# Performance work log

Hardware: AMD Instinct MI355X
Metric: run time of the kernel (lower is better)

Reference implementation:

```python
import jax, jax.numpy as jnp
import numpy as np

VERY_NEGATIVE_NUMBER = -1e30


def setup_inputs() -> dict:
    key = jax.random.key(0)
    ks = jax.random.split(key, 7)
    B, N, M, D = 16, 1024, 1024, 128
    inv_sqrt_d = 1.0 / np.sqrt(D).astype(np.float32)
    query = jax.random.normal(ks[0], (B, N, D), jnp.float32)
    memory = jax.random.normal(ks[1], (B, M, D), jnp.float32)
    # trilinear similarity parameters (BiDAF)
    w_q = jax.random.normal(ks[2], (D,), jnp.float32) * inv_sqrt_d
    w_m = jax.random.normal(ks[3], (D,), jnp.float32) * inv_sqrt_d
    w_qm = jax.random.normal(ks[4], (D,), jnp.float32) * inv_sqrt_d
    query_mask = jax.random.randint(ks[5], (B, N), 0, 2, jnp.int32)
    memory_mask = jax.random.randint(ks[6], (B, M), 0, 2, jnp.int32)
    return {
        "query": query,
        "memory": memory,
        "w_q": w_q,
        "w_m": w_m,
        "w_qm": w_qm,
        "query_mask": query_mask,
        "memory_mask": memory_mask,
    }


def reference(query, memory, w_q, w_m, w_qm, query_mask, memory_mask):
    # trilinear similarity: sim[b,n,m] = w_q.q_n + w_m.m_m + sum_d w_qm_d * q_nd * m_md
    sim = (
        jnp.einsum("bnd,d->bn", query, w_q)[:, :, None]
        + jnp.einsum("bmd,d->bm", memory, w_m)[:, None, :]
        + jnp.einsum("bnd,d,bmd->bnm", query, w_qm, memory)
    )  # [B, N, M]
    mask = (
        query_mask[:, :, None].astype(sim.dtype)
        * memory_mask[:, None, :].astype(sim.dtype)
    )  # [B, N, M]
    sim = sim + (1.0 - mask) * VERY_NEGATIVE_NUMBER
    # query -> memory attention (row-wise softmax over memory axis)
    q2m_prob = jax.nn.softmax(sim, axis=-1)  # [B, N, M]
    query_memory_attention = jnp.einsum("bnm,bmd->bnd", q2m_prob, memory)
    # memory -> query attention (softmax over row maxima, one vector per batch)
    m2q_prob = jax.nn.softmax(jnp.max(sim, axis=-1), axis=-1)  # [B, N]
    m2q = jnp.einsum("bn,bnd->bd", m2q_prob, query)[:, None, :]  # [B, 1, D]
    memory_query_attention = jnp.broadcast_to(m2q, query_memory_attention.shape)
    return (query_memory_attention, memory_query_attention)
```

## Files before the change

kernel.cpp:

```cpp
#include <hip/hip_runtime.h>
#include <hip/hip_bf16.h>
#include <stdint.h>

#define BB 16
#define NN 1024
#define MM 1024
#define DD 128
#define VERY_NEG (-1e30f)
#define LOG2E 1.44269504f
#define HALF_M 512
#define NCH 8

using bf16x8 = __attribute__((ext_vector_type(8))) short;
using f32x4  = __attribute__((ext_vector_type(4))) float;

__device__ inline unsigned short f2bf(float f) {
    union { float f; uint32_t u; } cv; cv.f = f;
    uint32_t u = cv.u;
    return (unsigned short)((u + 0x7FFFu + ((u >> 16) & 1u)) >> 16);
}
#define EXP2F(x) __builtin_amdgcn_exp2f(x)

typedef __attribute__((address_space(3))) unsigned int lds_u32;
typedef const __attribute__((address_space(1))) unsigned int glb_u32;
__device__ __forceinline__ void gl16(const void* g, void* l) {
    __builtin_amdgcn_global_load_lds((glb_u32*)g, (lds_u32*)l, 16, 0, 0);
}

__global__ void prep_rows(const float* __restrict__ q, const float* __restrict__ mem,
                          const float* __restrict__ wq, const float* __restrict__ wm,
                          const float* __restrict__ wqm, const int* __restrict__ mmask,
                          float* __restrict__ a, float* __restrict__ c1s,
                          unsigned short* __restrict__ qp, unsigned short* __restrict__ mb)
{
    int wave = (blockIdx.x * 256 + threadIdx.x) >> 6;
    int lane = threadIdx.x & 63;
    bool is_q = wave < BB * NN;
    int row = is_q ? wave : wave - BB * NN;
    const float* src = (is_q ? q : mem) + (size_t)row * DD;
    const float* wd  = is_q ? wq : wm;
    float2 v  = *(const float2*)(src + lane * 2);
    float2 w2 = *(const float2*)(wd + lane * 2);
    float dot = v.x * w2.x + v.y * w2.y;
    #pragma unroll
    for (int o = 32; o; o >>= 1) dot += __shfl_xor(dot, o);
    if (lane == 0) {
        if (is_q) a[row] = dot;
        else {
            int mm = mmask[row];
            c1s[row] = (dot + (mm ? 0.f : VERY_NEG)) * LOG2E;
        }
    }
    float2 s2 = v;
    if (is_q) {
        float2 wv = *(const float2*)(wqm + lane * 2);
        s2.x *= wv.x * LOG2E; s2.y *= wv.y * LOG2E;
    }
    ushort2 o2; o2.x = f2bf(s2.x); o2.y = f2bf(s2.y);
    *(ushort2*)((is_q ? qp : mb) + (size_t)row * DD + lane * 2) = o2;
}

__global__ void transpose_mem(const float* __restrict__ mem, unsigned short* __restrict__ mt)
{
    __shared__ unsigned short t[64][72];
    int bid = blockIdx.x;
    int dt = bid & 1, mtile = (bid >> 1) & 15, b = bid >> 5;
    int d0 = dt * 64, m0 = mtile * 64;
    int tid = threadIdx.x;
    int cc = tid & 63, rr = tid >> 6;
    #pragma unroll
    for (int r = 0; r < 64; r += 4) {
        float v = mem[((size_t)b * MM + m0 + r + rr) * DD + d0 + cc];
        t[cc][r + rr] = f2bf(v);
    }
    __syncthreads();
    #pragma unroll
    for (int r = 0; r < 64; r += 4) {
        mt[((size_t)b * DD + d0 + r + rr) * MM + m0 + cc] = t[r + rr][cc];
    }
}

__global__ __launch_bounds__(512) void flash_fwd(
    const unsigned short* __restrict__ qp, const unsigned short* __restrict__ mb,
    const unsigned short* __restrict__ mt,
    const float* __restrict__ a, const float* __restrict__ c1s,
    const int* __restrict__ qmask,
    float* __restrict__ out1, float* __restrict__ rowmax)
{
    __shared__ __align__(16) char smem[155648];
    unsigned short* KbBase = (unsigned short*)smem;
    unsigned short* VbBase = (unsigned short*)(smem + 65536);
    unsigned short (*pl)[16][72] = (unsigned short(*)[16][72])(smem + 131072);
    float* c1L = (float*)(smem + 149504);
    float (*mlb)[16][2] = (float(*)[16][2])(smem + 153600);
    float (*Obuf)[16][130] = (float(*)[16][130])smem;

    int tid = threadIdx.x;
    int w = tid >> 6, lane = tid & 63;
    int qt = w & 3, mh = w >> 2;
    int g = lane >> 4, qi = lane & 15;
    int b = blockIdx.x >> 4, nt = blockIdx.x & 15;
    int n0q = nt * 64 + qt * 16;

    const unsigned short* mbB = mb + (size_t)b * MM * DD;
    const unsigned short* mtB = mt + (size_t)b * DD * MM;

    {
        float2 cv = *(const float2*)(c1s + b * MM + tid * 2);
        *(float2*)&c1L[tid * 2] = cv;
    }

    const unsigned short* qpb = qp + ((size_t)b * NN + n0q) * DD;
    bf16x8 qf[4];
    #pragma unroll
    for (int kc = 0; kc < 4; kc++)
        qf[kc] = *(const bf16x8*)(qpb + qi * DD + kc * 32 + g * 8);

    float a_q = a[b * NN + n0q + qi];
    int   qm  = qmask[b * NN + n0q + qi];

    float m_run = -INFINITY, l_run = 0.f;
    f32x4 o[8];
    #pragma unroll
    for (int d2 = 0; d2 < 8; d2++) o[d2] = (f32x4){0.f, 0.f, 0.f, 0.f};

    auto stage = [&](int m0, unsigned short* Kc, unsigned short* Vc) {
        #pragma unroll
        for (int i = 0; i < 8; i++) {
            int j = qt * 8 + i;
            if (j < 16) {
                const unsigned short* gsrc = mbB
                    + (size_t)(m0 + (j >> 2) * 16 + (lane & 15)) * DD
                    + (j & 3) * 32 + (lane >> 4) * 8;
                gl16(gsrc, Kc + j * 512);
            } else {
                int j2 = j - 16;
                const unsigned short* gsrc = mtB
                    + (size_t)((j2 >> 1) * 16 + (lane & 15)) * MM
                    + m0 + (j2 & 1) * 32 + (lane >> 4) * 8;
                gl16(gsrc, Vc + j2 * 512);
            }
        }
    };
    auto Kbuf = [&](int bufi) { return KbBase + (mh * 2 + bufi) * 8192; };
    auto Vbuf = [&](int bufi) { return VbBase + (mh * 2 + bufi) * 8192; };

    stage(mh * HALF_M, Kbuf(0), Vbuf(0));
    __syncthreads();

    int cur = 0;
    for (int ch = 0; ch < NCH; ch++) {
        int m0 = mh * HALF_M + ch * 64;
        if (ch + 1 < NCH)
            stage(m0 + 64, Kbuf(cur ^ 1), Vbuf(cur ^ 1));

        const unsigned short* Kc = Kbuf(cur);
        const unsigned short* Vc = Vbuf(cur);

        f32x4 st[4];
        #pragma unroll
        for (int t = 0; t < 4; t++) st[t] = (f32x4){0, 0, 0, 0};
        #pragma unroll
        for (int t = 0; t < 4; t++) {
            #pragma unroll
            for (int kc = 0; kc < 4; kc++) {
                bf16x8 af = *(const bf16x8*)(Kc + ((t * 4 + kc) * 64 + lane) * 8);
                st[t] = __builtin_amdgcn_mfma_f32_16x16x32_bf16(af, qf[kc], st[t], 0, 0, 0);
            }
        }
        float sv[4][4];
        float cmax = -INFINITY;
        #pragma unroll
        for (int t = 0; t < 4; t++) {
            float4 c1v = *(const float4*)&c1L[m0 + t * 16 + g * 4];
            float cc4[4] = {c1v.x, c1v.y, c1v.z, c1v.w};
            #pragma unroll
            for (int i = 0; i < 4; i++) {
                float s = qm ? (st[t][i] + cc4[i]) : 0.f;
                sv[t][i] = s;
                cmax = fmaxf(cmax, s);
            }
        }
        cmax = fmaxf(cmax, __shfl_xor(cmax, 16));
        cmax = fmaxf(cmax, __shfl_xor(cmax, 32));
        float m_new = fmaxf(m_run, cmax);
        float alpha = EXP2F(m_run - m_new);
        float psum = 0.f;
        #pragma unroll
        for (int t = 0; t < 4; t++) {
            unsigned short pe[4];
            #pragma unroll
            for (int i = 0; i < 4; i++) {
                float p = EXP2F(sv[t][i] - m_new);
                psum += p;
                pe[i] = f2bf(p);
            }
            ushort4 pw2; pw2.x = pe[0]; pw2.y = pe[1]; pw2.z = pe[2]; pw2.w = pe[3];
            *(ushort4*)(&pl[w][qi][t * 16 + g * 4]) = pw2;
        }
        psum += __shfl_xor(psum, 16);
        psum += __shfl_xor(psum, 32);
        l_run = l_run * alpha + psum;
        m_run = m_new;

        float aL[4];
        #pragma unroll
        for (int i = 0; i < 4; i++) aL[i] = __shfl(alpha, g * 4 + i);

        __builtin_amdgcn_sched_barrier(0);
        bf16x8 pa0 = *(const bf16x8*)(&pl[w][qi][g * 8]);
        bf16x8 pa1 = *(const bf16x8*)(&pl[w][qi][32 + g * 8]);
        #pragma unroll
        for (int d2 = 0; d2 < 8; d2++) {
            bf16x8 vf0 = *(const bf16x8*)(Vc + ((d2 * 2 + 0) * 64 + lane) * 8);
            bf16x8 vf1 = *(const bf16x8*)(Vc + ((d2 * 2 + 1) * 64 + lane) * 8);
            f32x4 oo = o[d2];
            #pragma unroll
            for (int i = 0; i < 4; i++) oo[i] *= aL[i];
            oo = __builtin_amdgcn_mfma_f32_16x16x32_bf16(pa0, vf0, oo, 0, 0, 0);
            o[d2] = __builtin_amdgcn_mfma_f32_16x16x32_bf16(pa1, vf1, oo, 0, 0, 0);
        }

        __syncthreads();
        cur ^= 1;
    }

    if (g == 0) { mlb[w][qi][0] = m_run; mlb[w][qi][1] = l_run; }
    __syncthreads();
    int pw = w ^ 4;
    float mo[4], mp[4];
    #pragma unroll
    for (int i = 0; i < 4; i++) {
        int r = g * 4 + i;
        mo[i] = __shfl(m_run, r);
        mp[i] = mlb[pw][r][0];
    }
    if (mh == 0) {
        #pragma unroll
        for (int i = 0; i < 4; i++) {
            float M = fmaxf(mo[i], mp[i]);
            float wsc = EXP2F(mo[i] - M);
            #pragma unroll
            for (int d2 = 0; d2 < 8; d2++)
                Obuf[qt][g * 4 + i][d2 * 16 + qi] = o[d2][i] * wsc;
        }
    }
    __syncthreads();
    if (mh == 1) {
        #pragma unroll
        for (int i = 0; i < 4; i++) {
            int r = g * 4 + i;
            float M = fmaxf(mo[i], mp[i]);
            float ws1 = EXP2F(mo[i] - M);
            float lo = __shfl(l_run, r);
            float lg = mlb[pw][r][1] * EXP2F(mp[i] - M) + lo * ws1;
            float invl = 1.f / lg;
            #pragma unroll
            for (int d2 = 0; d2 < 8; d2++) {
                float val = (Obuf[qt][r][d2 * 16 + qi] + o[d2][i] * ws1) * invl;
                out1[((size_t)b * NN + n0q + r) * DD + d2 * 16 + qi] = val;
            }
        }
        if (g == 0) {
            float M = fmaxf(m_run, mlb[pw][qi][0]);
            rowmax[b * NN + n0q + qi] = M * (1.f / LOG2E) + a_q + (qm ? 0.f : VERY_NEG);
        }
    }
}

__global__ __launch_bounds__(256) void m2q_partial(
    const float* __restrict__ rowmax, const float* __restrict__ query,
    float* __restrict__ partial, float* __restrict__ Zbuf)
{
    int bid = blockIdx.x;
    int b = bid >> 3, ch = bid & 7;
    int tid = threadIdx.x, lane = tid & 63, wv = tid >> 6;
    __shared__ float red[8];
    __shared__ float pe[128];
    __shared__ float acc1[128];

    float4 rv = *(const float4*)(rowmax + b * NN + tid * 4);
    float mx = fmaxf(fmaxf(rv.x, rv.y), fmaxf(rv.z, rv.w));
    #pragma unroll
    for (int o = 32; o; o >>= 1) mx = fmaxf(mx, __shfl_xor(mx, o));
    if (lane == 0) red[wv] = mx;
    __syncthreads();
    mx = fmaxf(fmaxf(red[0], red[1]), fmaxf(red[2], red[3]));
    float ls = __expf(rv.x - mx) + __expf(rv.y - mx) + __expf(rv.z - mx) + __expf(rv.w - mx);
    #pragma unroll
    for (int o = 32; o; o >>= 1) ls += __shfl_xor(ls, o);
    if (lane == 0) red[4 + wv] = ls;
    if (tid < 128) pe[tid] = __expf(rowmax[b * NN + ch * 128 + tid] - mx);
    __syncthreads();
    float Z = (red[4] + red[5]) + (red[6] + red[7]);

    int d = tid & 127, h = tid >> 7;
    const float* qb = query + ((size_t)b * NN + ch * 128 + h * 64) * DD + d;
    float acc = 0.f;
    #pragma unroll 8
    for (int n = 0; n < 64; n++) acc += pe[h * 64 + n] * qb[(size_t)n * DD];
    if (h) acc1[d] = acc;
    __syncthreads();
    if (!h) partial[(b * 8 + ch) * DD + d] = acc + acc1[d];
    if (tid == 0) Zbuf[b] = Z;
}

__global__ __launch_bounds__(256) void bcast_kernel(
    const float* __restrict__ partial, const float* __restrict__ Zbuf,
    float4* __restrict__ out2)
{
    __shared__ float m2qL[128];
    int i = blockIdx.x * 256 + threadIdx.x;
    int b = i >> 15;
    int tid = threadIdx.x;
    if (tid < 128) {
        float s = 0.f;
        #pragma unroll
        for (int ch = 0; ch < 8; ch++) s += partial[(b * 8 + ch) * DD + tid];
        m2qL[tid] = s / Zbuf[b];
    }
    __syncthreads();
    out2[i] = ((const float4*)m2qL)[i & 31];
}

extern "C" void kernel_launch(void* const* d_in, const int* in_sizes, int n_in,
                              void* d_out, int out_size, void* d_ws, size_t ws_size,
                              hipStream_t stream)
{
    const float* query  = (const float*)d_in[0];
    const float* memory = (const float*)d_in[1];
    const float* w_q    = (const float*)d_in[2];
    const float* w_m    = (const float*)d_in[3];
    const float* w_qm   = (const float*)d_in[4];
    const int*   qmask  = (const int*)d_in[5];
    const int*   mmask  = (const int*)d_in[6];
    float* out1 = (float*)d_out;
    float* out2 = out1 + (size_t)BB * NN * DD;

    char* ws = (char*)d_ws;
    float* a       = (float*)ws;
    float* c1s     = a + BB * NN;
    float* rowmax  = c1s + BB * MM;
    float* partial = rowmax + BB * NN;
    float* Zbuf    = partial + BB * 8 * DD;
    unsigned short* qp = (unsigned short*)(ws + (1 << 20));
    unsigned short* mb = qp + (size_t)BB * NN * DD;
    unsigned short* mt = mb + (size_t)BB * MM * DD;

    prep_rows<<<dim3((BB * NN + BB * MM) / 4), 256, 0, stream>>>(query, memory, w_q, w_m, w_qm, mmask, a, c1s, qp, mb);
    transpose_mem<<<dim3(BB * (MM / 64) * (DD / 64)), 256, 0, stream>>>(memory, mt);
    flash_fwd<<<dim3(BB * 16), 512, 0, stream>>>(qp, mb, mt, a, c1s, qmask, out1, rowmax);
    m2q_partial<<<dim3(BB * 8), 256, 0, stream>>>(rowmax, query, partial, Zbuf);
    bcast_kernel<<<dim3(2048), 256, 0, stream>>>(partial, Zbuf, (float4*)out2);
}
```

Before: 55.48 us.

## Fuse prep kernels and restructure flash attention to per-wave staging with two query tiles

Merges the row-prep and memory-transpose kernels into one launch to cut a kernel launch. The flash kernel drops from 512 to 256 threads per block. Each wave now handles two 16-row query tiles against 32-wide memory chunks, so each K/V fragment loaded from LDS feeds two MFMAs. Each wave double-buffers its own K/V in private LDS, and an explicit vmcnt wait replaces the per-chunk block barrier. m2q_partial is split into 16 chunks per batch to add parallelism. The risks are fewer waves to hide latency and more register pressure from the doubled accumulators.

```diff
diff --git a/kernel.cpp b/kernel.cpp
--- a/kernel.cpp
+++ b/kernel.cpp
@@ -8,8 +8,7 @@
 #define DD 128
 #define VERY_NEG (-1e30f)
 #define LOG2E 1.44269504f
-#define HALF_M 512
-#define NCH 8
+#define NCH 16
 
 using bf16x8 = __attribute__((ext_vector_type(8))) short;
 using f32x4  = __attribute__((ext_vector_type(4))) float;
@@ -27,243 +26,273 @@
     __builtin_amdgcn_global_load_lds((glb_u32*)g, (lds_u32*)l, 16, 0, 0);
 }
 
-__global__ void prep_rows(const float* __restrict__ q, const float* __restrict__ mem,
-                          const float* __restrict__ wq, const float* __restrict__ wm,
-                          const float* __restrict__ wqm, const int* __restrict__ mmask,
-                          float* __restrict__ a, float* __restrict__ c1s,
-                          unsigned short* __restrict__ qp, unsigned short* __restrict__ mb)
-{
-    int wave = (blockIdx.x * 256 + threadIdx.x) >> 6;
-    int lane = threadIdx.x & 63;
-    bool is_q = wave < BB * NN;
-    int row = is_q ? wave : wave - BB * NN;
-    const float* src = (is_q ? q : mem) + (size_t)row * DD;
-    const float* wd  = is_q ? wq : wm;
-    float2 v  = *(const float2*)(src + lane * 2);
-    float2 w2 = *(const float2*)(wd + lane * 2);
-    float dot = v.x * w2.x + v.y * w2.y;
-    #pragma unroll
-    for (int o = 32; o; o >>= 1) dot += __shfl_xor(dot, o);
-    if (lane == 0) {
-        if (is_q) a[row] = dot;
-        else {
-            int mm = mmask[row];
-            c1s[row] = (dot + (mm ? 0.f : VERY_NEG)) * LOG2E;
-        }
-    }
-    float2 s2 = v;
-    if (is_q) {
-        float2 wv = *(const float2*)(wqm + lane * 2);
-        s2.x *= wv.x * LOG2E; s2.y *= wv.y * LOG2E;
-    }
-    ushort2 o2; o2.x = f2bf(s2.x); o2.y = f2bf(s2.y);
-    *(ushort2*)((is_q ? qp : mb) + (size_t)row * DD + lane * 2) = o2;
-}
-
-__global__ void transpose_mem(const float* __restrict__ mem, unsigned short* __restrict__ mt)
+__global__ __launch_bounds__(256) void prep_all(
+    const float* __restrict__ q, const float* __restrict__ mem,
+    const float* __restrict__ wq, const float* __restrict__ wm,
+    const float* __restrict__ wqm, const int* __restrict__ mmask,
+    float* __restrict__ a, float* __restrict__ c1s,
+    unsigned short* __restrict__ qp, unsigned short* __restrict__ mb,
+    unsigned short* __restrict__ mt)
 {
     __shared__ unsigned short t[64][72];
-    int bid = blockIdx.x;
-    int dt = bid & 1, mtile = (bid >> 1) & 15, b = bid >> 5;
-    int d0 = dt * 64, m0 = mtile * 64;
-    int tid = threadIdx.x;
-    int cc = tid & 63, rr = tid >> 6;
-    #pragma unroll
-    for (int r = 0; r < 64; r += 4) {
-        float v = mem[((size_t)b * MM + m0 + r + rr) * DD + d0 + cc];
-        t[cc][r + rr] = f2bf(v);
-    }
-    __syncthreads();
-    #pragma unroll
-    for (int r = 0; r < 64; r += 4) {
-        mt[((size_t)b * DD + d0 + r + rr) * MM + m0 + cc] = t[r + rr][cc];
-    }
-}
-
-__global__ __launch_bounds__(512) void flash_fwd(
+    if (blockIdx.x < 8192) {
+        int wave = (blockIdx.x * 256 + threadIdx.x) >> 6;
+        int lane = threadIdx.x & 63;
+        bool is_q = wave < BB * NN;
+        int row = is_q ? wave : wave - BB * NN;
+        const float* src = (is_q ? q : mem) + (size_t)row * DD;
+        const float* wd  = is_q ? wq : wm;
+        float2 v  = *(const float2*)(src + lane * 2);
+        float2 w2 = *(const float2*)(wd + lane * 2);
+        float dot = v.x * w2.x + v.y * w2.y;
+        #pragma unroll
+        for (int o = 32; o; o >>= 1) dot += __shfl_xor(dot, o);
+        if (lane == 0) {
+            if (is_q) a[row] = dot;
+            else {
+                int mm = mmask[row];
+                c1s[row] = (dot + (mm ? 0.f : VERY_NEG)) * LOG2E;
+            }
+        }
+        float2 s2 = v;
+        if (is_q) {
+            float2 wv = *(const float2*)(wqm + lane * 2);
+            s2.x *= wv.x * LOG2E; s2.y *= wv.y * LOG2E;
+        }
+        ushort2 o2; o2.x = f2bf(s2.x); o2.y = f2bf(s2.y);
+        *(ushort2*)((is_q ? qp : mb) + (size_t)row * DD + lane * 2) = o2;
+    } else {
+        int bid = blockIdx.x - 8192;
+        int dt = bid & 1, mtile = (bid >> 1) & 15, b = bid >> 5;
+        int d0 = dt * 64, m0 = mtile * 64;
+        int tid = threadIdx.x;
+        int cc = tid & 63, rr = tid >> 6;
+        #pragma unroll
+        for (int r = 0; r < 64; r += 4) {
+            float v = mem[((size_t)b * MM + m0 + r + rr) * DD + d0 + cc];
+            t[cc][r + rr] = f2bf(v);
+        }
+        __syncthreads();
+        #pragma unroll
+        for (int r = 0; r < 64; r += 4) {
+            mt[((size_t)b * DD + d0 + r + rr) * MM + m0 + cc] = t[r + rr][cc];
+        }
+    }
+}
+
+__global__ __launch_bounds__(256) void flash_fwd(
     const unsigned short* __restrict__ qp, const unsigned short* __restrict__ mb,
     const unsigned short* __restrict__ mt,
     const float* __restrict__ a, const float* __restrict__ c1s,
     const int* __restrict__ qmask,
     float* __restrict__ out1, float* __restrict__ rowmax)
 {
-    __shared__ __align__(16) char smem[155648];
-    unsigned short* KbBase = (unsigned short*)smem;
-    unsigned short* VbBase = (unsigned short*)(smem + 65536);
-    unsigned short (*pl)[16][72] = (unsigned short(*)[16][72])(smem + 131072);
-    float* c1L = (float*)(smem + 149504);
-    float (*mlb)[16][2] = (float(*)[16][2])(smem + 153600);
+    __shared__ __align__(16) char smem[146432];
+    unsigned short* stg = (unsigned short*)smem;
+    unsigned short (*pl)[2][16][40] = (unsigned short(*)[2][16][40])(smem + 131072);
+    float* c1L = (float*)(smem + 141312);
+    float (*mlb)[2][16][2] = (float(*)[2][16][2])(smem + 145408);
     float (*Obuf)[16][130] = (float(*)[16][130])smem;
 
     int tid = threadIdx.x;
     int w = tid >> 6, lane = tid & 63;
-    int qt = w & 3, mh = w >> 2;
+    int qw = w & 1, mh = w >> 1;
     int g = lane >> 4, qi = lane & 15;
     int b = blockIdx.x >> 4, nt = blockIdx.x & 15;
-    int n0q = nt * 64 + qt * 16;
+    int n0q = nt * 64 + qw * 32;
 
     const unsigned short* mbB = mb + (size_t)b * MM * DD;
     const unsigned short* mtB = mt + (size_t)b * DD * MM;
 
     {
-        float2 cv = *(const float2*)(c1s + b * MM + tid * 2);
-        *(float2*)&c1L[tid * 2] = cv;
+        float4 cv = *(const float4*)(c1s + b * MM + tid * 4);
+        *(float4*)&c1L[tid * 4] = cv;
     }
 
     const unsigned short* qpb = qp + ((size_t)b * NN + n0q) * DD;
-    bf16x8 qf[4];
-    #pragma unroll
-    for (int kc = 0; kc < 4; kc++)
-        qf[kc] = *(const bf16x8*)(qpb + qi * DD + kc * 32 + g * 8);
-
-    float a_q = a[b * NN + n0q + qi];
-    int   qm  = qmask[b * NN + n0q + qi];
-
-    float m_run = -INFINITY, l_run = 0.f;
-    f32x4 o[8];
-    #pragma unroll
-    for (int d2 = 0; d2 < 8; d2++) o[d2] = (f32x4){0.f, 0.f, 0.f, 0.f};
-
-    auto stage = [&](int m0, unsigned short* Kc, unsigned short* Vc) {
-        #pragma unroll
-        for (int i = 0; i < 8; i++) {
-            int j = qt * 8 + i;
-            if (j < 16) {
-                const unsigned short* gsrc = mbB
-                    + (size_t)(m0 + (j >> 2) * 16 + (lane & 15)) * DD
-                    + (j & 3) * 32 + (lane >> 4) * 8;
-                gl16(gsrc, Kc + j * 512);
-            } else {
-                int j2 = j - 16;
-                const unsigned short* gsrc = mtB
-                    + (size_t)((j2 >> 1) * 16 + (lane & 15)) * MM
-                    + m0 + (j2 & 1) * 32 + (lane >> 4) * 8;
-                gl16(gsrc, Vc + j2 * 512);
-            }
+    bf16x8 qf[2][4];
+    #pragma unroll
+    for (int qt = 0; qt < 2; qt++)
+        #pragma unroll
+        for (int kc = 0; kc < 4; kc++)
+            qf[qt][kc] = *(const bf16x8*)(qpb + (qt * 16 + qi) * DD + kc * 32 + g * 8);
+
+    float a_q[2]; int qm[2];
+    #pragma unroll
+    for (int qt = 0; qt < 2; qt++) {
+        a_q[qt] = a[b * NN + n0q + qt * 16 + qi];
+        qm[qt]  = qmask[b * NN + n0q + qt * 16 + qi];
+    }
+
+    float m_run[2] = {-INFINITY, -INFINITY}, l_run[2] = {0.f, 0.f};
+    f32x4 o[2][8];
+    #pragma unroll
+    for (int qt = 0; qt < 2; qt++)
+        #pragma unroll
+        for (int d2 = 0; d2 < 8; d2++) o[qt][d2] = (f32x4){0.f, 0.f, 0.f, 0.f};
+
+    auto stage = [&](int m0, unsigned short* buf) {
+        #pragma unroll
+        for (int j = 0; j < 8; j++) {
+            const unsigned short* gsrc = mbB
+                + (size_t)(m0 + (j >> 2) * 16 + qi) * DD + (j & 3) * 32 + g * 8;
+            gl16(gsrc, buf + j * 512);
+        }
+        #pragma unroll
+        for (int d2 = 0; d2 < 8; d2++) {
+            const unsigned short* gsrc = mtB
+                + (size_t)(d2 * 16 + qi) * MM + m0 + g * 8;
+            gl16(gsrc, buf + (8 + d2) * 512);
         }
     };
-    auto Kbuf = [&](int bufi) { return KbBase + (mh * 2 + bufi) * 8192; };
-    auto Vbuf = [&](int bufi) { return VbBase + (mh * 2 + bufi) * 8192; };
-
-    stage(mh * HALF_M, Kbuf(0), Vbuf(0));
+    unsigned short* buf0 = stg + (w * 2 + 0) * 8192;
+    unsigned short* buf1 = stg + (w * 2 + 1) * 8192;
+
+    int mbase = mh * (MM / 2);
+    stage(mbase, buf0);
     __syncthreads();
 
     int cur = 0;
     for (int ch = 0; ch < NCH; ch++) {
-        int m0 = mh * HALF_M + ch * 64;
-        if (ch + 1 < NCH)
-            stage(m0 + 64, Kbuf(cur ^ 1), Vbuf(cur ^ 1));
-
-        const unsigned short* Kc = Kbuf(cur);
-        const unsigned short* Vc = Vbuf(cur);
-
-        f32x4 st[4];
-        #pragma unroll
-        for (int t = 0; t < 4; t++) st[t] = (f32x4){0, 0, 0, 0};
-        #pragma unroll
-        for (int t = 0; t < 4; t++) {
+        int m0 = mbase + ch * 32;
+        unsigned short* bc = cur ? buf1 : buf0;
+        unsigned short* bn = cur ? buf0 : buf1;
+        if (ch + 1 < NCH) {
+            stage(m0 + 32, bn);
+            asm volatile("s_waitcnt vmcnt(16)" ::: "memory");
+        } else {
+            asm volatile("s_waitcnt vmcnt(0)" ::: "memory");
+        }
+        __builtin_amdgcn_sched_barrier(0);
+
+        f32x4 st[2][2];
+        #pragma unroll
+        for (int qt = 0; qt < 2; qt++) { st[qt][0] = (f32x4){0,0,0,0}; st[qt][1] = (f32x4){0,0,0,0}; }
+        #pragma unroll
+        for (int t = 0; t < 2; t++) {
             #pragma unroll
             for (int kc = 0; kc < 4; kc++) {
-                bf16x8 af = *(const bf16x8*)(Kc + ((t * 4 + kc) * 64 + lane) * 8);
-                st[t] = __builtin_amdgcn_mfma_f32_16x16x32_bf16(af, qf[kc], st[t], 0, 0, 0);
-            }
-        }
-        float sv[4][4];
-        float cmax = -INFINITY;
-        #pragma unroll
-        for (int t = 0; t < 4; t++) {
-            float4 c1v = *(const float4*)&c1L[m0 + t * 16 + g * 4];
-            float cc4[4] = {c1v.x, c1v.y, c1v.z, c1v.w};
-            #pragma unroll
-            for (int i = 0; i < 4; i++) {
-                float s = qm ? (st[t][i] + cc4[i]) : 0.f;
-                sv[t][i] = s;
-                cmax = fmaxf(cmax, s);
-            }
-        }
-        cmax = fmaxf(cmax, __shfl_xor(cmax, 16));
-        cmax = fmaxf(cmax, __shfl_xor(cmax, 32));
-        float m_new = fmaxf(m_run, cmax);
-        float alpha = EXP2F(m_run - m_new);
-        float psum = 0.f;
-        #pragma unroll
-        for (int t = 0; t < 4; t++) {
-            unsigned short pe[4];
-            #pragma unroll
-            for (int i = 0; i < 4; i++) {
-                float p = EXP2F(sv[t][i] - m_new);
-                psum += p;
-                pe[i] = f2bf(p);
-            }
-            ushort4 pw2; pw2.x = pe[0]; pw2.y = pe[1]; pw2.z = pe[2]; pw2.w = pe[3];
-            *(ushort4*)(&pl[w][qi][t * 16 + g * 4]) = pw2;
-        }
-        psum += __shfl_xor(psum, 16);
-        psum += __shfl_xor(psum, 32);
-        l_run = l_run * alpha + psum;
-        m_run = m_new;
-
-        float aL[4];
-        #pragma unroll
-        for (int i = 0; i < 4; i++) aL[i] = __shfl(alpha, g * 4 + i);
+                bf16x8 af = *(const bf16x8*)(bc + ((t * 4 + kc) * 64 + lane) * 8);
+                #pragma unroll
+                for (int qt = 0; qt < 2; qt++)
+                    st[qt][t] = __builtin_amdgcn_mfma_f32_16x16x32_bf16(af, qf[qt][kc], st[qt][t], 0, 0, 0);
+            }
+        }
+        float aL[2][4];
+        #pragma unroll
+        for (int qt = 0; qt < 2; qt++) {
+            float sv[2][4];
+            float cmax = -INFINITY;
+            #pragma unroll
+            for (int t = 0; t < 2; t++) {
+                float4 c1v = *(const float4*)&c1L[m0 + t * 16 + g * 4];
+                float cc4[4] = {c1v.x, c1v.y, c1v.z, c1v.w};
+                #pragma unroll
+                for (int i = 0; i < 4; i++) {
+                    float s = qm[qt] ? (st[qt][t][i] + cc4[i]) : 0.f;
+                    sv[t][i] = s;
+                    cmax = fmaxf(cmax, s);
+                }
+            }
+            cmax = fmaxf(cmax, __shfl_xor(cmax, 16));
+            cmax = fmaxf(cmax, __shfl_xor(cmax, 32));
+            float m_new = fmaxf(m_run[qt], cmax);
+            float alpha = EXP2F(m_run[qt] - m_new);
+            float psum = 0.f;
+            #pragma unroll
+            for (int t = 0; t < 2; t++) {
+                unsigned short pe[4];
+                #pragma unroll
+                for (int i = 0; i < 4; i++) {
+                    float p = EXP2F(sv[t][i] - m_new);
+                    psum += p;
+                    pe[i] = f2bf(p);
+                }
+                ushort4 pw2; pw2.x = pe[0]; pw2.y = pe[1]; pw2.z = pe[2]; pw2.w = pe[3];
+                *(ushort4*)(&pl[w][qt][qi][t * 16 + g * 4]) = pw2;
+            }
+            psum += __shfl_xor(psum, 16);
+            psum += __shfl_xor(psum, 32);
+            l_run[qt] = l_run[qt] * alpha + psum;
+            m_run[qt] = m_new;
+            #pragma unroll
+            for (int i = 0; i < 4; i++) aL[qt][i] = __shfl(alpha, g * 4 + i);
+        }
 
         __builtin_amdgcn_sched_barrier(0);
-        bf16x8 pa0 = *(const bf16x8*)(&pl[w][qi][g * 8]);
-        bf16x8 pa1 = *(const bf16x8*)(&pl[w][qi][32 + g * 8]);
+        bf16x8 pa[2];
+        pa[0] = *(const bf16x8*)(&pl[w][0][qi][g * 8]);
+        pa[1] = *(const bf16x8*)(&pl[w][1][qi][g * 8]);
         #pragma unroll
         for (int d2 = 0; d2 < 8; d2++) {
-            bf16x8 vf0 = *(const bf16x8*)(Vc + ((d2 * 2 + 0) * 64 + lane) * 8);
-            bf16x8 vf1 = *(const bf16x8*)(Vc + ((d2 * 2 + 1) * 64 + lane) * 8);
-            f32x4 oo = o[d2];
-            #pragma unroll
-            for (int i = 0; i < 4; i++) oo[i] *= aL[i];
-            oo = __builtin_amdgcn_mfma_f32_16x16x32_bf16(pa0, vf0, oo, 0, 0, 0);
-            o[d2] = __builtin_amdgcn_mfma_f32_16x16x32_bf16(pa1, vf1, oo, 0, 0, 0);
-        }
-
-        __syncthreads();
+            bf16x8 vf = *(const bf16x8*)(bc + ((8 + d2) * 64 + lane) * 8);
+            #pragma unroll
+            for (int qt = 0; qt < 2; qt++) {
+                f32x4 oo = o[qt][d2];
+                #pragma unroll
+                for (int i = 0; i < 4; i++) oo[i] *= aL[qt][i];
+                o[qt][d2] = __builtin_amdgcn_mfma_f32_16x16x32_bf16(pa[qt], vf, oo, 0, 0, 0);
+            }
+        }
         cur ^= 1;
     }
 
-    if (g == 0) { mlb[w][qi][0] = m_run; mlb[w][qi][1] = l_run; }
-    __syncthreads();
-    int pw = w ^ 4;
-    float mo[4], mp[4];
-    #pragma unroll
-    for (int i = 0; i < 4; i++) {
-        int r = g * 4 + i;
-        mo[i] = __shfl(m_run, r);
-        mp[i] = mlb[pw][r][0];
-    }
-    if (mh == 0) {
-        #pragma unroll
-        for (int i = 0; i < 4; i++) {
-            float M = fmaxf(mo[i], mp[i]);
-            float wsc = EXP2F(mo[i] - M);
-            #pragma unroll
-            for (int d2 = 0; d2 < 8; d2++)
-                Obuf[qt][g * 4 + i][d2 * 16 + qi] = o[d2][i] * wsc;
-        }
-    }
-    __syncthreads();
-    if (mh == 1) {
+    if (g == 0) {
+        #pragma unroll
+        for (int qt = 0; qt < 2; qt++) { mlb[w][qt][qi][0] = m_run[qt]; mlb[w][qt][qi][1] = l_run[qt]; }
+    }
+    __syncthreads();
+    int pw = w ^ 2;
+    #pragma unroll
+    for (int qt = 0; qt < 2; qt++) {
+        float mo[4], mp[4];
         #pragma unroll
         for (int i = 0; i < 4; i++) {
             int r = g * 4 + i;
-            float M = fmaxf(mo[i], mp[i]);
-            float ws1 = EXP2F(mo[i] - M);
-            float lo = __shfl(l_run, r);
-            float lg = mlb[pw][r][1] * EXP2F(mp[i] - M) + lo * ws1;
-            float invl = 1.f / lg;
-            #pragma unroll
-            for (int d2 = 0; d2 < 8; d2++) {
-                float val = (Obuf[qt][r][d2 * 16 + qi] + o[d2][i] * ws1) * invl;
-                out1[((size_t)b * NN + n0q + r) * DD + d2 * 16 + qi] = val;
-            }
-        }
-        if (g == 0) {
-            float M = fmaxf(m_run, mlb[pw][qi][0]);
-            rowmax[b * NN + n0q + qi] = M * (1.f / LOG2E) + a_q + (qm ? 0.f : VERY_NEG);
+            mo[i] = __shfl(m_run[qt], r);
+            mp[i] = mlb[pw][qt][r][0];
+        }
+        if (mh == 0) {
+            #pragma unroll
+            for (int i = 0; i < 4; i++) {
+                float M = fmaxf(mo[i], mp[i]);
+                float wsc = EXP2F(mo[i] - M);
+                #pragma unroll
+                for (int d2 = 0; d2 < 8; d2++)
+                    Obuf[qw * 2 + qt][g * 4 + i][d2 * 16 + qi] = o[qt][d2][i] * wsc;
+            }
+        }
+    }
+    __syncthreads();
+    if (mh == 1) {
+        #pragma unroll
+        for (int qt = 0; qt < 2; qt++) {
+            float mo[4], mp[4];
+            #pragma unroll
+            for (int i = 0; i < 4; i++) {
+                int r = g * 4 + i;
+                mo[i] = __shfl(m_run[qt], r);
+                mp[i] = mlb[pw][qt][r][0];
+            }
+            #pragma unroll
+            for (int i = 0; i < 4; i++) {
+                int r = g * 4 + i;
+                float M = fmaxf(mo[i], mp[i]);
+                float ws1 = EXP2F(mo[i] - M);
+                float lo = __shfl(l_run[qt], r);
+                float lg = mlb[pw][qt][r][1] * EXP2F(mp[i] - M) + lo * ws1;
+                float invl = 1.f / lg;
+                #pragma unroll
+                for (int d2 = 0; d2 < 8; d2++) {
+                    float val = (Obuf[qw * 2 + qt][r][d2 * 16 + qi] + o[qt][d2][i] * ws1) * invl;
+                    out1[((size_t)b * NN + n0q + qt * 16 + r) * DD + d2 * 16 + qi] = val;
+                }
+            }
+            if (g == 0) {
+                float M = fmaxf(m_run[qt], mlb[pw][qt][qi][0]);
+                rowmax[b * NN + n0q + qt * 16 + qi] =
+                    M * (1.f / LOG2E) + a_q[qt] + (qm[qt] ? 0.f : VERY_NEG);
+            }
         }
     }
 }
@@ -273,10 +302,10 @@
     float* __restrict__ partial, float* __restrict__ Zbuf)
 {
     int bid = blockIdx.x;
-    int b = bid >> 3, ch = bid & 7;
+    int b = bid >> 4, ch = bid & 15;
     int tid = threadIdx.x, lane = tid & 63, wv = tid >> 6;
     __shared__ float red[8];
-    __shared__ float pe[128];
+    __shared__ float pe[64];
     __shared__ float acc1[128];
 
     float4 rv = *(const float4*)(rowmax + b * NN + tid * 4);
@@ -290,18 +319,18 @@
     #pragma unroll
     for (int o = 32; o; o >>= 1) ls += __shfl_xor(ls, o);
     if (lane == 0) red[4 + wv] = ls;
-    if (tid < 128) pe[tid] = __expf(rowmax[b * NN + ch * 128 + tid] - mx);
+    if (tid < 64) pe[tid] = __expf(rowmax[b * NN + ch * 64 + tid] - mx);
     __syncthreads();
     float Z = (red[4] + red[5]) + (red[6] + red[7]);
 
     int d = tid & 127, h = tid >> 7;
-    const float* qb = query + ((size_t)b * NN + ch * 128 + h * 64) * DD + d;
+    const float* qb = query + ((size_t)b * NN + ch * 64 + h * 32) * DD + d;
     float acc = 0.f;
     #pragma unroll 8
-    for (int n = 0; n < 64; n++) acc += pe[h * 64 + n] * qb[(size_t)n * DD];
+    for (int n = 0; n < 32; n++) acc += pe[h * 32 + n] * qb[(size_t)n * DD];
     if (h) acc1[d] = acc;
     __syncthreads();
-    if (!h) partial[(b * 8 + ch) * DD + d] = acc + acc1[d];
+    if (!h) partial[(b * 16 + ch) * DD + d] = acc + acc1[d];
     if (tid == 0) Zbuf[b] = Z;
 }
 
@@ -316,7 +345,7 @@
     if (tid < 128) {
         float s = 0.f;
         #pragma unroll
-        for (int ch = 0; ch < 8; ch++) s += partial[(b * 8 + ch) * DD + tid];
+        for (int ch = 0; ch < 16; ch++) s += partial[(b * 16 + ch) * DD + tid];
         m2qL[tid] = s / Zbuf[b];
     }
     __syncthreads();
@@ -342,14 +371,14 @@
     float* c1s     = a + BB * NN;
     float* rowmax  = c1s + BB * MM;
     float* partial = rowmax + BB * NN;
-    float* Zbuf    = partial + BB * 8 * DD;
+    float* Zbuf    = partial + BB * 16 * DD;
     unsigned short* qp = (unsigned short*)(ws + (1 << 20));
     unsigned short* mb = qp + (size_t)BB * NN * DD;
     unsigned short* mt = mb + (size_t)BB * MM * DD;
 
-    prep_rows<<<dim3((BB * NN + BB * MM) / 4), 256, 0, stream>>>(query, memory, w_q, w_m, w_qm, mmask, a, c1s, qp, mb);
-    transpose_mem<<<dim3(BB * (MM / 64) * (DD / 64)), 256, 0, stream>>>(memory, mt);
-    flash_fwd<<<dim3(BB * 16), 512, 0, stream>>>(qp, mb, mt, a, c1s, qmask, out1, rowmax);
-    m2q_partial<<<dim3(BB * 8), 256, 0, stream>>>(rowmax, query, partial, Zbuf);
+    prep_all<<<dim3(8192 + 512), 256, 0, stream>>>(query, memory, w_q, w_m, w_qm, mmask,
+                                                   a, c1s, qp, mb, mt);
+    flash_fwd<<<dim3(BB * 16), 256, 0, stream>>>(qp, mb, mt, a, c1s, qmask, out1, rowmax);
+    m2q_partial<<<dim3(BB * 16), 256, 0, stream>>>(rowmax, query, partial, Zbuf);
     bcast_kernel<<<dim3(2048), 256, 0, stream>>>(partial, Zbuf, (float4*)out2);
 }
```

New measurement: 64.95 us. 17.1% more time.
